# Kernel optimization log

Measured on AMD Instinct MI355X. Metric: run time of the kernel, lower is better.

The kernel has to match this reference:

```python
import jax, jax.numpy as jnp
import numpy as np

K = 4
G = 64
IN_DIM = 256
OUT_DIM = 256
BATCH = 512
T0, T1 = -1.0, 1.0


def setup_inputs() -> dict:
    key = jax.random.key(0)
    kx, kw = jax.random.split(key)
    x = jax.random.uniform(kx, (BATCH, IN_DIM), jnp.float32, T0, T1)
    # xavier_normal_ on [G+K, in, out]: std = sqrt(2 / (fan_in + fan_out)) with fan over last two dims
    std = (2.0 / (IN_DIM + OUT_DIM)) ** 0.5
    w = jax.random.normal(kw, (G + K, IN_DIM, OUT_DIM), jnp.float32) * std
    # knot vector: k-1 repeats of t0, linspace(t0,t1,G+1), k-1 repeats of t1
    t = jnp.concatenate([
        jnp.full((K - 1,), T0, jnp.float32),
        jnp.linspace(T0, T1, G + 1, dtype=jnp.float32),
        jnp.full((K - 1,), T1, jnp.float32),
    ])
    return {"x": x, "w": w, "t": t, "k": K}


def _basis(x, t, k):
    """Cox-de Boor: the k nonzero order-k B-spline basis values at each x.
    Returns (idx, N): idx [..., k] basis indices i-k+1..i, N [..., k] values."""
    n_t = t.shape[0]
    # interval i with t[i] <= x < t[i+1], clipped to the valid span
    i = jnp.clip(jnp.searchsorted(t, x, side='right') - 1, k - 1, n_t - k - 1)
    N = jnp.ones(x.shape + (1,), x.dtype)
    for p in range(1, k):  # static small loop (k=4)
        jj = jnp.arange(1, p + 1)
        left = x[..., None] - t[i[..., None] + 1 - jj]   # [..., p]
        right = t[i[..., None] + jj] - x[..., None]      # [..., p]
        saved = jnp.zeros_like(x)
        vals = []
        for r in range(p):
            d = right[..., r] + left[..., p - 1 - r]      # t[i+r+1] - t[i+r+1-p]
            temp = N[..., r] / d
            vals.append(saved + right[..., r] * temp)
            saved = left[..., p - 1 - r] * temp
        vals.append(saved)
        N = jnp.stack(vals, -1)
    idx = i[..., None] - (k - 1) + jnp.arange(k)
    return idx, N


def reference(x, w, t, k):
    in_dim = x.shape[1]
    n_rows = w.shape[0]
    idx, y1 = _basis(x, t, k)                             # [B,in,k], [B,in,k]
    # last row of w (index -1 == n_rows-1) weights the SiLU residual term
    idx_full = jnp.concatenate(
        [idx, jnp.full(idx.shape[:-1] + (1,), n_rows - 1, idx.dtype)], -1)  # [B,in,k+1]
    silu = x * jax.nn.sigmoid(x)
    y2 = jnp.concatenate([y1, silu[..., None]], -1)       # [B,in,k+1]
    # gather local spline coefficients: w2[b,c,j,o] = w[idx_full[b,c,j], c, o]
    w2 = w[idx_full, jnp.arange(in_dim)[None, :, None], :]  # [B,in,k+1,out]
    return jnp.einsum('bcjo,bcj->bo', w2, y2)             # [B,out]
```

## Files before the change

### kernel.cpp

```cpp
#include <hip/hip_runtime.h>
#include <math.h>
#include <stdint.h>

#define IN_DIM  256
#define OUT_DIM 256
#define NROWS   68
#define NT      71
#define BATCH   512
#define W_ELEMS (NROWS * IN_DIM * OUT_DIM)
#define NCG     32
#define PART_FLOATS (NCG * BATCH * OUT_DIM)

__device__ __forceinline__ uint32_t bf16_rne(float f) {
  uint32_t u = __builtin_bit_cast(uint32_t, f);
  return (u + 0x7fffu + ((u >> 16) & 1u)) >> 16;
}

__global__ __launch_bounds__(256) void cvt_kernel(const float* __restrict__ w,
                                                  uint32_t* __restrict__ wb) {
  const int base = (blockIdx.x * 256 + threadIdx.x) * 8;
  const float4 a = *(const float4*)(w + base);
  const float4 b = *(const float4*)(w + base + 4);
  uint4 o;
  o.x = bf16_rne(a.x) | (bf16_rne(a.y) << 16);
  o.y = bf16_rne(a.z) | (bf16_rne(a.w) << 16);
  o.z = bf16_rne(b.x) | (bf16_rne(b.y) << 16);
  o.w = bf16_rne(b.z) | (bf16_rne(b.w) << 16);
  *(uint4*)(wb + base / 2) = o;
}

__device__ __forceinline__ void fma8(const uint4 q, const float y, float* acc) {
  acc[0] += y * __builtin_bit_cast(float, q.x << 16);
  acc[1] += y * __builtin_bit_cast(float, q.x & 0xffff0000u);
  acc[2] += y * __builtin_bit_cast(float, q.y << 16);
  acc[3] += y * __builtin_bit_cast(float, q.y & 0xffff0000u);
  acc[4] += y * __builtin_bit_cast(float, q.z << 16);
  acc[5] += y * __builtin_bit_cast(float, q.z & 0xffff0000u);
  acc[6] += y * __builtin_bit_cast(float, q.w << 16);
  acc[7] += y * __builtin_bit_cast(float, q.w & 0xffff0000u);
}

__global__ __launch_bounds__(256) void kan_gather_kernel(
    const float* __restrict__ x, const uint4* __restrict__ wp,
    const float* __restrict__ t, float* __restrict__ part) {
  __shared__ float  lt[NT];
  __shared__ float4 nA[8][32];
  __shared__ float  sA[8][32];
  __shared__ int    bA[8][32];

  const int tid = threadIdx.x;
  const unsigned bid = blockIdx.x;
  const int cg     = bid & 31;
  const int bgroup = bid >> 5;

  if (tid < NT) lt[tid] = t[tid];
  __syncthreads();

  {
    const int cl = tid & 7;
    const int bb = tid >> 3;
    const float xv = x[(size_t)(bgroup * 32 + bb) * IN_DIM + cg * 8 + cl];
    int i = 3 + (int)floorf((xv + 1.0f) * 32.0f);
    i = i < 3 ? 3 : (i > 66 ? 66 : i);
    while (i > 3 && xv < lt[i]) --i;
    while (i < 66 && xv >= lt[i + 1]) ++i;

    float N0 = 1.f, N1 = 0.f, N2 = 0.f, N3 = 0.f;
    {
      const float l1 = xv - lt[i];
      const float r1 = lt[i + 1] - xv;
      const float tp = N0 / (r1 + l1);
      N1 = l1 * tp; N0 = r1 * tp;
    }
    {
      const float l1 = xv - lt[i];
      const float l2 = xv - lt[i - 1];
      const float r1 = lt[i + 1] - xv;
      const float r2 = lt[i + 2] - xv;
      float saved = 0.f;
      const float tp0 = N0 / (r1 + l2);
      const float n0 = saved + r1 * tp0; saved = l2 * tp0;
      const float tp1 = N1 / (r2 + l1);
      const float n1 = saved + r2 * tp1; saved = l1 * tp1;
      N0 = n0; N1 = n1; N2 = saved;
    }
    {
      const float l1 = xv - lt[i];
      const float l2 = xv - lt[i - 1];
      const float l3 = xv - lt[i - 2];
      const float r1 = lt[i + 1] - xv;
      const float r2 = lt[i + 2] - xv;
      const float r3 = lt[i + 3] - xv;
      float saved = 0.f;
      const float tp0 = N0 / (r1 + l3);
      const float n0 = saved + r1 * tp0; saved = l3 * tp0;
      const float tp1 = N1 / (r2 + l2);
      const float n1 = saved + r2 * tp1; saved = l2 * tp1;
      const float tp2 = N2 / (r3 + l1);
      const float n2 = saved + r3 * tp2; saved = l1 * tp2;
      N0 = n0; N1 = n1; N2 = n2; N3 = saved;
    }
    nA[cl][bb] = make_float4(N0, N1, N2, N3);
    sA[cl][bb] = xv / (1.0f + expf(-xv));
    bA[cl][bb] = i - 3;
  }
  __syncthreads();

  const int wv   = tid >> 6;
  const int lane = tid & 63;
  const int half = lane >> 5;
  const int ol   = lane & 31;

  float acc[4][8];
  #pragma unroll
  for (int p = 0; p < 4; ++p) {
    #pragma unroll
    for (int j = 0; j < 8; ++j) acc[p][j] = 0.f;
  }

  for (int ch = 0; ch < 8; ++ch) {
    const uint32_t cbase = (uint32_t)((cg * 8 + ch) * 32 + ol);
    const uint4 q4 = wp[cbase + 67u * 8192u];

    uint4 q[4][4];
    #pragma unroll
    for (int p = 0; p < 4; ++p) {
      const int bb = wv * 8 + p * 2 + half;
      const uint32_t rb = cbase + ((uint32_t)bA[ch][bb] << 13);
      q[p][0] = wp[rb];
      q[p][1] = wp[rb +  8192u];
      q[p][2] = wp[rb + 16384u];
      q[p][3] = wp[rb + 24576u];
    }
    #pragma unroll
    for (int p = 0; p < 4; ++p) {
      const int bb = wv * 8 + p * 2 + half;
      const float4 yv = nA[ch][bb];
      const float  ys = sA[ch][bb];
      fma8(q[p][0], yv.x, acc[p]);
      fma8(q[p][1], yv.y, acc[p]);
      fma8(q[p][2], yv.z, acc[p]);
      fma8(q[p][3], yv.w, acc[p]);
      fma8(q4,      ys,   acc[p]);
    }
    __syncthreads();
  }

  {
    float* dst0 = part + ((size_t)cg * BATCH + bgroup * 32) * OUT_DIM;
    #pragma unroll
    for (int p = 0; p < 4; ++p) {
      const int bb = wv * 8 + p * 2 + half;
      float* d = dst0 + (size_t)bb * OUT_DIM + ol * 8;
      *(float4*)d       = make_float4(acc[p][0], acc[p][1], acc[p][2], acc[p][3]);
      *(float4*)(d + 4) = make_float4(acc[p][4], acc[p][5], acc[p][6], acc[p][7]);
    }
  }
}

__global__ __launch_bounds__(256) void reduce_kernel(const float* __restrict__ part,
                                                     float* __restrict__ out) {
  const int q = blockIdx.x * 256 + threadIdx.x;
  const int S = BATCH * OUT_DIM / 4;
  const float4* p = (const float4*)part;
  float4 s = p[q];
  #pragma unroll
  for (int k = 1; k < NCG; ++k) {
    const float4 a = p[q + k * S];
    s.x += a.x; s.y += a.y; s.z += a.z; s.w += a.w;
  }
  ((float4*)out)[q] = s;
}

extern "C" void kernel_launch(void* const* d_in, const int* in_sizes, int n_in,
                              void* d_out, int out_size, void* d_ws, size_t ws_size,
                              hipStream_t stream) {
  const float* x = (const float*)d_in[0];
  const float* w = (const float*)d_in[1];
  const float* t = (const float*)d_in[2];
  float* out  = (float*)d_out;
  float* part = (float*)d_ws;
  uint32_t* wb = (uint32_t*)d_ws + PART_FLOATS;
  cvt_kernel<<<W_ELEMS / (256 * 8), 256, 0, stream>>>(w, wb);
  kan_gather_kernel<<<512, 256, 0, stream>>>(x, (const uint4*)wb, t, part);
  reduce_kernel<<<BATCH * OUT_DIM / 4 / 256, 256, 0, stream>>>(part, out);
}
```

Baseline: 94.07 us.

## Recast spline gather as dense fp16 MFMA over padded knot dimension

Result: slower. 100.1 us (+6.4%).

```diff
diff --git a/kernel.cpp b/kernel.cpp
--- a/kernel.cpp
+++ b/kernel.cpp
@@ -1,4 +1,5 @@
 #include <hip/hip_runtime.h>
+#include <hip/hip_fp16.h>
 #include <math.h>
 #include <stdint.h>
 
@@ -7,154 +8,175 @@
 #define NROWS   68
 #define NT      71
 #define BATCH   512
-#define W_ELEMS (NROWS * IN_DIM * OUT_DIM)
+#define KPAD    96
 #define NCG     32
 #define PART_FLOATS (NCG * BATCH * OUT_DIM)
-
-__device__ __forceinline__ uint32_t bf16_rne(float f) {
-  uint32_t u = __builtin_bit_cast(uint32_t, f);
-  return (u + 0x7fffu + ((u >> 16) & 1u)) >> 16;
-}
+#define WB_SHORTS   (IN_DIM * OUT_DIM * KPAD)
+
+typedef _Float16 f16x8 __attribute__((ext_vector_type(8)));
+typedef float    f32x4 __attribute__((ext_vector_type(4)));
 
 __global__ __launch_bounds__(256) void cvt_kernel(const float* __restrict__ w,
-                                                  uint32_t* __restrict__ wb) {
-  const int base = (blockIdx.x * 256 + threadIdx.x) * 8;
-  const float4 a = *(const float4*)(w + base);
-  const float4 b = *(const float4*)(w + base + 4);
-  uint4 o;
-  o.x = bf16_rne(a.x) | (bf16_rne(a.y) << 16);
-  o.y = bf16_rne(a.z) | (bf16_rne(a.w) << 16);
-  o.z = bf16_rne(b.x) | (bf16_rne(b.y) << 16);
-  o.w = bf16_rne(b.z) | (bf16_rne(b.w) << 16);
-  *(uint4*)(wb + base / 2) = o;
-}
-
-__device__ __forceinline__ void fma8(const uint4 q, const float y, float* acc) {
-  acc[0] += y * __builtin_bit_cast(float, q.x << 16);
-  acc[1] += y * __builtin_bit_cast(float, q.x & 0xffff0000u);
-  acc[2] += y * __builtin_bit_cast(float, q.y << 16);
-  acc[3] += y * __builtin_bit_cast(float, q.y & 0xffff0000u);
-  acc[4] += y * __builtin_bit_cast(float, q.z << 16);
-  acc[5] += y * __builtin_bit_cast(float, q.z & 0xffff0000u);
-  acc[6] += y * __builtin_bit_cast(float, q.w << 16);
-  acc[7] += y * __builtin_bit_cast(float, q.w & 0xffff0000u);
+                                                  unsigned short* __restrict__ wb) {
+  __shared__ unsigned short l16[NROWS][64];
+  const int c  = blockIdx.x >> 2;
+  const int ot = (blockIdx.x & 3) << 6;
+  const int t  = threadIdx.x;
+  const int o1 = t & 63, k0 = t >> 6;
+  for (int k = k0; k < NROWS; k += 4) {
+    const float v = w[((size_t)k * IN_DIM + c) * OUT_DIM + ot + o1];
+    l16[k][o1] = __half_as_ushort(__float2half_rn(v));
+  }
+  __syncthreads();
+  #pragma unroll
+  for (int i = 0; i < 3; ++i) {
+    const int u = t + 256 * i;
+    const int o2 = u / 12, seg = u % 12, k8 = seg * 8;
+    uint32_t hl[4];
+    #pragma unroll
+    for (int j = 0; j < 4; ++j) {
+      const int ka = k8 + 2 * j, kb = ka + 1;
+      const uint32_t lo = (ka < NROWS) ? l16[ka][o2] : 0u;
+      const uint32_t hi = (kb < NROWS) ? l16[kb][o2] : 0u;
+      hl[j] = lo | (hi << 16);
+    }
+    *(uint4*)(wb + ((size_t)(c * 256 + ot + o2) * KPAD + k8)) =
+        make_uint4(hl[0], hl[1], hl[2], hl[3]);
+  }
 }
 
 __global__ __launch_bounds__(256) void kan_gather_kernel(
-    const float* __restrict__ x, const uint4* __restrict__ wp,
+    const float* __restrict__ x, const unsigned short* __restrict__ wbu,
     const float* __restrict__ t, float* __restrict__ part) {
+  __shared__ uint4 Wb[2][3072];
+  __shared__ unsigned short Ylds[64 * 104];
+  __shared__ float4 nA[8][64];
+  __shared__ float  sA[8][64];
+  __shared__ int    bA[8][64];
   __shared__ float  lt[NT];
-  __shared__ float4 nA[8][32];
-  __shared__ float  sA[8][32];
-  __shared__ int    bA[8][32];
-
-  const int tid = threadIdx.x;
-  const unsigned bid = blockIdx.x;
-  const int cg     = bid & 31;
-  const int bgroup = bid >> 5;
+
+  const int tid   = threadIdx.x;
+  const int cg    = blockIdx.x & 31;
+  const int btile = blockIdx.x >> 5;
+  const int wv    = tid >> 6;
+  const int lane  = tid & 63;
+  const int m16   = lane & 15;
+  const int g16b  = (lane >> 4) * 16;
 
   if (tid < NT) lt[tid] = t[tid];
   __syncthreads();
 
   {
-    const int cl = tid & 7;
-    const int bb = tid >> 3;
-    const float xv = x[(size_t)(bgroup * 32 + bb) * IN_DIM + cg * 8 + cl];
+    const char* src0 = (const char*)wbu + (size_t)(cg * 8 + 0) * 49152;
+    #pragma unroll
+    for (int j = 0; j < 12; ++j) {
+      const int s = wv * 12 + j;
+      __builtin_amdgcn_global_load_lds((const uint32_t*)(src0 + s * 1024 + lane * 16),
+                                       (uint32_t*)(&Wb[0][s * 64]), 16, 0, 0);
+    }
+  }
+
+  for (int p = tid; p < 512; p += 256) {
+    const int c = p >> 6, bb = p & 63;
+    const float xv = x[(size_t)(btile * 64 + bb) * IN_DIM + cg * 8 + c];
     int i = 3 + (int)floorf((xv + 1.0f) * 32.0f);
     i = i < 3 ? 3 : (i > 66 ? 66 : i);
     while (i > 3 && xv < lt[i]) --i;
     while (i < 66 && xv >= lt[i + 1]) ++i;
-
     float N0 = 1.f, N1 = 0.f, N2 = 0.f, N3 = 0.f;
-    {
-      const float l1 = xv - lt[i];
-      const float r1 = lt[i + 1] - xv;
-      const float tp = N0 / (r1 + l1);
-      N1 = l1 * tp; N0 = r1 * tp;
-    }
-    {
-      const float l1 = xv - lt[i];
-      const float l2 = xv - lt[i - 1];
-      const float r1 = lt[i + 1] - xv;
-      const float r2 = lt[i + 2] - xv;
+    { const float l1 = xv - lt[i], r1 = lt[i + 1] - xv;
+      const float tp = N0 / (r1 + l1); N1 = l1 * tp; N0 = r1 * tp; }
+    { const float l1 = xv - lt[i], l2 = xv - lt[i - 1];
+      const float r1 = lt[i + 1] - xv, r2 = lt[i + 2] - xv;
       float saved = 0.f;
-      const float tp0 = N0 / (r1 + l2);
-      const float n0 = saved + r1 * tp0; saved = l2 * tp0;
-      const float tp1 = N1 / (r2 + l1);
-      const float n1 = saved + r2 * tp1; saved = l1 * tp1;
-      N0 = n0; N1 = n1; N2 = saved;
-    }
-    {
-      const float l1 = xv - lt[i];
-      const float l2 = xv - lt[i - 1];
-      const float l3 = xv - lt[i - 2];
-      const float r1 = lt[i + 1] - xv;
-      const float r2 = lt[i + 2] - xv;
-      const float r3 = lt[i + 3] - xv;
+      const float tp0 = N0 / (r1 + l2); const float n0 = saved + r1 * tp0; saved = l2 * tp0;
+      const float tp1 = N1 / (r2 + l1); const float n1 = saved + r2 * tp1; saved = l1 * tp1;
+      N0 = n0; N1 = n1; N2 = saved; }
+    { const float l1 = xv - lt[i], l2 = xv - lt[i - 1], l3 = xv - lt[i - 2];
+      const float r1 = lt[i + 1] - xv, r2 = lt[i + 2] - xv, r3 = lt[i + 3] - xv;
       float saved = 0.f;
-      const float tp0 = N0 / (r1 + l3);
-      const float n0 = saved + r1 * tp0; saved = l3 * tp0;
-      const float tp1 = N1 / (r2 + l2);
-      const float n1 = saved + r2 * tp1; saved = l2 * tp1;
-      const float tp2 = N2 / (r3 + l1);
-      const float n2 = saved + r3 * tp2; saved = l1 * tp2;
-      N0 = n0; N1 = n1; N2 = n2; N3 = saved;
-    }
-    nA[cl][bb] = make_float4(N0, N1, N2, N3);
-    sA[cl][bb] = xv / (1.0f + expf(-xv));
-    bA[cl][bb] = i - 3;
-  }
-  __syncthreads();
-
-  const int wv   = tid >> 6;
-  const int lane = tid & 63;
-  const int half = lane >> 5;
-  const int ol   = lane & 31;
-
-  float acc[4][8];
-  #pragma unroll
-  for (int p = 0; p < 4; ++p) {
-    #pragma unroll
-    for (int j = 0; j < 8; ++j) acc[p][j] = 0.f;
-  }
+      const float tp0 = N0 / (r1 + l3); const float n0 = saved + r1 * tp0; saved = l3 * tp0;
+      const float tp1 = N1 / (r2 + l2); const float n1 = saved + r2 * tp1; saved = l2 * tp1;
+      const float tp2 = N2 / (r3 + l1); const float n2 = saved + r3 * tp2; saved = l1 * tp2;
+      N0 = n0; N1 = n1; N2 = n2; N3 = saved; }
+    nA[c][bb] = make_float4(N0, N1, N2, N3);
+    sA[c][bb] = xv / (1.0f + expf(-xv));
+    bA[c][bb] = i - 3;
+  }
+  __syncthreads();
+
+  f32x4 acc[4][4];
+  #pragma unroll
+  for (int a = 0; a < 4; ++a)
+    #pragma unroll
+    for (int b = 0; b < 4; ++b) acc[a][b] = f32x4{0.f, 0.f, 0.f, 0.f};
 
   for (int ch = 0; ch < 8; ++ch) {
-    const uint32_t cbase = (uint32_t)((cg * 8 + ch) * 32 + ol);
-    const uint4 q4 = wp[cbase + 67u * 8192u];
-
-    uint4 q[4][4];
-    #pragma unroll
-    for (int p = 0; p < 4; ++p) {
-      const int bb = wv * 8 + p * 2 + half;
-      const uint32_t rb = cbase + ((uint32_t)bA[ch][bb] << 13);
-      q[p][0] = wp[rb];
-      q[p][1] = wp[rb +  8192u];
-      q[p][2] = wp[rb + 16384u];
-      q[p][3] = wp[rb + 24576u];
-    }
-    #pragma unroll
-    for (int p = 0; p < 4; ++p) {
-      const int bb = wv * 8 + p * 2 + half;
+    for (int i = tid; i < 1664; i += 256)
+      *(uint2*)((char*)Ylds + (size_t)i * 8) = make_uint2(0u, 0u);
+    __syncthreads();
+    if (tid < 64) {
+      const int bb = tid;
+      unsigned short* yr = &Ylds[bb * 104];
       const float4 yv = nA[ch][bb];
-      const float  ys = sA[ch][bb];
-      fma8(q[p][0], yv.x, acc[p]);
-      fma8(q[p][1], yv.y, acc[p]);
-      fma8(q[p][2], yv.z, acc[p]);
-      fma8(q[p][3], yv.w, acc[p]);
-      fma8(q4,      ys,   acc[p]);
+      const int base = bA[ch][bb];
+      yr[base + 0] = __half_as_ushort(__float2half_rn(yv.x));
+      yr[base + 1] = __half_as_ushort(__float2half_rn(yv.y));
+      yr[base + 2] = __half_as_ushort(__float2half_rn(yv.z));
+      yr[base + 3] = __half_as_ushort(__float2half_rn(yv.w));
+      yr[67]       = __half_as_ushort(__float2half_rn(sA[ch][bb]));
     }
     __syncthreads();
-  }
-
-  {
-    float* dst0 = part + ((size_t)cg * BATCH + bgroup * 32) * OUT_DIM;
-    #pragma unroll
-    for (int p = 0; p < 4; ++p) {
-      const int bb = wv * 8 + p * 2 + half;
-      float* d = dst0 + (size_t)bb * OUT_DIM + ol * 8;
-      *(float4*)d       = make_float4(acc[p][0], acc[p][1], acc[p][2], acc[p][3]);
-      *(float4*)(d + 4) = make_float4(acc[p][4], acc[p][5], acc[p][6], acc[p][7]);
-    }
+
+    if (ch < 7) {
+      const char* srcN = (const char*)wbu + (size_t)(cg * 8 + ch + 1) * 49152;
+      uint4* dstN = &Wb[(ch + 1) & 1][0];
+      #pragma unroll
+      for (int j = 0; j < 12; ++j) {
+        const int s = wv * 12 + j;
+        __builtin_amdgcn_global_load_lds((const uint32_t*)(srcN + s * 1024 + lane * 16),
+                                         (uint32_t*)(dstN + s * 64), 16, 0, 0);
+      }
+    }
+
+    const char* Wc = (const char*)&Wb[ch & 1][0];
+    #pragma unroll
+    for (int kb = 0; kb < 3; ++kb) {
+      f16x8 af[4];
+      #pragma unroll
+      for (int ot = 0; ot < 4; ++ot) {
+        const int o = wv * 64 + ot * 16 + m16;
+        af[ot] = *(const f16x8*)(Wc + o * 192 + kb * 64 + g16b);
+      }
+      #pragma unroll
+      for (int bt = 0; bt < 4; ++bt) {
+        const f16x8 bf = *(const f16x8*)((const char*)Ylds + (bt * 16 + m16) * 208 + kb * 64 + g16b);
+        #pragma unroll
+        for (int ot = 0; ot < 4; ++ot)
+          acc[ot][bt] = __builtin_amdgcn_mfma_f32_16x16x32_f16(af[ot], bf, acc[ot][bt], 0, 0, 0);
+      }
+    }
+    __syncthreads();
+  }
+
+  float* bounce = (float*)&Wb[0][0];
+  #pragma unroll
+  for (int ot = 0; ot < 4; ++ot)
+    #pragma unroll
+    for (int bt = 0; bt < 4; ++bt)
+      #pragma unroll
+      for (int r = 0; r < 4; ++r) {
+        const int o = wv * 64 + ot * 16 + (lane >> 4) * 4 + r;
+        const int b = bt * 16 + m16;
+        bounce[b * 260 + o] = acc[ot][bt][r];
+      }
+  __syncthreads();
+  #pragma unroll
+  for (int i = 0; i < 16; ++i) {
+    const int idx = tid + 256 * i;
+    const int b = idx >> 6, o4 = (idx & 63) * 4;
+    const float4 v = *(const float4*)&bounce[b * 260 + o4];
+    *(float4*)(part + ((size_t)cg * BATCH + btile * 64 + b) * OUT_DIM + o4) = v;
   }
 }
 
@@ -180,8 +202,8 @@
   const float* t = (const float*)d_in[2];
   float* out  = (float*)d_out;
   float* part = (float*)d_ws;
-  uint32_t* wb = (uint32_t*)d_ws + PART_FLOATS;
-  cvt_kernel<<<W_ELEMS / (256 * 8), 256, 0, stream>>>(w, wb);
-  kan_gather_kernel<<<512, 256, 0, stream>>>(x, (const uint4*)wb, t, part);
+  unsigned short* wb = (unsigned short*)((float*)d_ws + PART_FLOATS);
+  cvt_kernel<<<1024, 256, 0, stream>>>(w, wb);
+  kan_gather_kernel<<<256, 256, 0, stream>>>(x, wb, t, part);
   reduce_kernel<<<BATCH * OUT_DIM / 4 / 256, 256, 0, stream>>>(part, out);
 }
```
